# Kernel optimization log

Measured on AMD Instinct MI355X. Metric: run time of the kernel, lower is better.

## Reference

```python
import jax, jax.numpy as jnp
import numpy as np

N = 100000   # nodes
E = 1600000  # edges
D_IN, D_H, D_OUT = 128, 256, 128
EPS = 1e-5


def _linear_params(key, fan_in, fan_out):
    lim = 1.0 / np.sqrt(fan_in)
    kw, kb = jax.random.split(key)
    W = jax.random.uniform(kw, (fan_in, fan_out), minval=-lim, maxval=lim, dtype=jnp.float32)
    b = jax.random.uniform(kb, (fan_out,), minval=-lim, maxval=lim, dtype=jnp.float32)
    return W, b


def setup_inputs() -> dict:
    key = jax.random.key(0)
    ks = jax.random.split(key, 8)
    W1, b1 = _linear_params(ks[0], D_IN, D_H)
    W2, b2 = _linear_params(ks[1], D_H, D_H)
    W3, b3 = _linear_params(ks[2], D_H, D_OUT)
    return {
        'feat': jax.random.normal(ks[3], (N, D_IN), dtype=jnp.float32),
        'W1': W1, 'b1': b1, 'g1': jnp.ones(D_H, jnp.float32), 'be1': jnp.zeros(D_H, jnp.float32), 'a1': jnp.full((1,), 0.25, jnp.float32),
        'W2': W2, 'b2': b2, 'g2': jnp.ones(D_H, jnp.float32), 'be2': jnp.zeros(D_H, jnp.float32), 'a2': jnp.full((1,), 0.25, jnp.float32),
        'W3': W3, 'b3': b3,
        'src': jax.random.randint(ks[4], (E,), 0, N, dtype=jnp.int32),
        'dst': jax.random.randint(ks[5], (E,), 0, N, dtype=jnp.int32),
    }


def _layer_norm(x, g, b):
    mu = jnp.mean(x, axis=-1, keepdims=True)
    var = jnp.mean((x - mu) ** 2, axis=-1, keepdims=True)
    return g * (x - mu) / jnp.sqrt(var + EPS) + b


def _prelu(x, a):
    return jnp.where(x >= 0, x, a * x)


def reference(feat, W1, b1, g1, be1, a1, W2, b2, g2, be2, a2, W3, b3, src, dst):
    ones = jnp.ones((E,), jnp.float32)
    # out-degree (of src nodes) and in-degree (of dst nodes), clamped to >= 1
    deg_out = jnp.maximum(jax.ops.segment_sum(ones, src, num_segments=N), 1.0) ** -0.5  # [N]
    deg_in = jnp.maximum(jax.ops.segment_sum(ones, dst, num_segments=N), 1.0) ** -0.5   # [N]

    def conv(h, W, b, g=None, be=None, a=None):
        x = h * deg_out[:, None]                                   # src-side degree norm
        agg = jax.ops.segment_sum(x[src], dst, num_segments=N)     # sparse sum aggregation
        r = (agg @ W + b) * deg_in[:, None]                        # linear + dst-side norm
        if g is not None:
            r = _prelu(_layer_norm(r, g, be), a)
        return r

    h = conv(feat, W1, b1, g1, be1, a1)
    h = conv(h, W2, b2, g2, be2, a2)
    h = conv(h, W3, b3)  # last layer: encoding=False -> no norm, no activation
    return h
```

## Files before the change

kernel.cpp:

```cpp
#include <hip/hip_runtime.h>
#include <cstdint>
#include <cstddef>

static constexpr int NN = 100000;
static constexpr int NE = 1600000;
static constexpr int NP = 100096;

static constexpr int NBUCK  = 391;
static constexpr int BCAP   = 5120;
static constexpr int NBUCKD = 782;
static constexpr int BCAPD  = 2816;
static constexpr int SCAP   = 448;
static constexpr int PBLK   = 200;
static constexpr int EPB    = 8000;

typedef __attribute__((ext_vector_type(8))) short short8;
typedef __attribute__((ext_vector_type(8))) unsigned short ushort8;
typedef __attribute__((ext_vector_type(4))) float f32x4;

__device__ inline ushort bf16_rtn(float x) {
    uint32_t u = __float_as_uint(x);
    uint32_t r = u + 0x7fffu + ((u >> 16) & 1u);
    return (ushort)(r >> 16);
}
__device__ inline float bf16_to_f(ushort u) {
    return __uint_as_float((uint32_t)u << 16);
}

__global__ __launch_bounds__(256) void k_init_cur(int* __restrict__ curA) {
    int b = blockIdx.x * 256 + threadIdx.x;
    if (b < NBUCK) curA[b] = b * BCAP;
}

__global__ __launch_bounds__(256) void k_partA(const int* __restrict__ src, const int* __restrict__ dst,
                                               int* __restrict__ curA, int* __restrict__ pairA) {
    __shared__ int hs[NBUCK];
    int e0 = blockIdx.x * EPB;
    for (int i = threadIdx.x; i < NBUCK; i += 256) hs[i] = 0;
    __syncthreads();
    for (int e = e0 + (int)threadIdx.x; e < e0 + EPB; e += 256)
        atomicAdd(&hs[src[e] >> 8], 1);
    __syncthreads();
    for (int i = threadIdx.x; i < NBUCK; i += 256) {
        int c = hs[i];
        hs[i] = c ? atomicAdd(&curA[i], c) : 0;
    }
    __syncthreads();
    for (int e = e0 + (int)threadIdx.x; e < e0 + EPB; e += 256) {
        int s = src[e], d = dst[e];
        int p = atomicAdd(&hs[s >> 8], 1);
        pairA[p] = (d << 8) | (s & 255);
    }
}

__global__ __launch_bounds__(256) void k_degout(const int* __restrict__ curA, const int* __restrict__ pairA,
                                                float* __restrict__ deg_out_inv) {
    __shared__ int h[256];
    int b = blockIdx.x;
    int p0 = b * BCAP;
    int n = curA[b] - p0;
    h[threadIdx.x] = 0;
    __syncthreads();
    for (int i = threadIdx.x; i < n; i += 256)
        atomicAdd(&h[pairA[p0 + i] & 255], 1);
    __syncthreads();
    int node = b * 256 + (int)threadIdx.x;
    if (node < NN)
        deg_out_inv[node] = rsqrtf(fmaxf((float)h[threadIdx.x], 1.0f));
}

__global__ __launch_bounds__(256) void k_countB(const int* __restrict__ curA, const int* __restrict__ pairA,
                                                int* __restrict__ cntB) {
    __shared__ int h[NBUCKD];
    int s = blockIdx.x;
    int p0 = s * BCAP;
    int n = curA[s] - p0;
    for (int i = threadIdx.x; i < NBUCKD; i += 256) h[i] = 0;
    __syncthreads();
    for (int i = threadIdx.x; i < n; i += 256)
        atomicAdd(&h[pairA[p0 + i] >> 15], 1);
    __syncthreads();
    for (int i = threadIdx.x; i < NBUCKD; i += 256)
        cntB[s * NBUCKD + i] = h[i];
}

__global__ __launch_bounds__(512) void k_scanB(const int* __restrict__ cntB, int* __restrict__ offB,
                                               int* __restrict__ fillB) {
    __shared__ int sd[512];
    int b = blockIdx.x;
    int t = threadIdx.x;
    int v = (t < NBUCK) ? cntB[t * NBUCKD + b] : 0;
    sd[t] = v;
    __syncthreads();
    #pragma unroll
    for (int off = 1; off < 512; off <<= 1) {
        int x = (t >= off) ? sd[t - off] : 0;
        __syncthreads();
        sd[t] += x;
        __syncthreads();
    }
    if (t < NBUCK) offB[t * NBUCKD + b] = b * BCAPD + sd[t] - v;
    if (t == NBUCK - 1) fillB[b] = sd[t];
}

__global__ __launch_bounds__(256) void k_placeB(const int* __restrict__ curA, const int* __restrict__ pairA,
                                                const int* __restrict__ offB, int* __restrict__ pairB) {
    __shared__ int cur[NBUCKD];
    int s = blockIdx.x;
    int p0 = s * BCAP;
    int n = curA[s] - p0;
    for (int i = threadIdx.x; i < NBUCKD; i += 256) cur[i] = offB[s * NBUCKD + i];
    __syncthreads();
    int sbase = s << 8;
    for (int i = threadIdx.x; i < n; i += 256) {
        int pk = pairA[p0 + i];
        int d = pk >> 8;
        int sfull = sbase | (pk & 255);
        int pos = atomicAdd(&cur[d >> 7], 1);
        pairB[pos] = (sfull << 7) | (d & 127);
    }
}

__global__ __launch_bounds__(256) void k_deg_in(const int* __restrict__ fillB, const int* __restrict__ pairB,
                                                float* __restrict__ deg_in_inv) {
    __shared__ int h[128];
    int b = blockIdx.x;
    int p0 = b * BCAPD;
    int n = fillB[b];
    if (threadIdx.x < 128) h[threadIdx.x] = 0;
    __syncthreads();
    for (int i = threadIdx.x; i < n; i += 256)
        atomicAdd(&h[pairB[p0 + i] & 127], 1);
    __syncthreads();
    if (threadIdx.x < 128) {
        int node = b * 128 + (int)threadIdx.x;
        deg_in_inv[node] = rsqrtf(fmaxf((float)h[threadIdx.x], 1.0f));
    }
}

__global__ __launch_bounds__(512) void k_split8(const int* __restrict__ fillB, const int* __restrict__ pairB,
                                                int* __restrict__ pairB2, int* __restrict__ fillS) {
    int b = blockIdx.x;
    int w = threadIdx.x >> 6;
    int l = threadIdx.x & 63;
    int n = fillB[b];
    const int* ep = pairB + (size_t)b * BCAPD;
    int* op = pairB2 + (size_t)(b * 8 + w) * SCAP;
    int cnt = 0;
    for (int i0 = 0; i0 < n; i0 += 64) {
        int idx = i0 + l;
        int pk = (idx < n) ? ep[idx] : 0;
        bool match = (idx < n) && ((pk & 7) == w);
        unsigned long long mask = __ballot(match);
        if (match) {
            int pos = __popcll(mask & ((1ull << l) - 1ull));
            op[cnt + pos] = pk;
        }
        cnt += __popcll(mask);
    }
    if (l == 0) fillS[b * 8 + w] = cnt;
}

__global__ __launch_bounds__(256) void k_cvt(const float* __restrict__ feat,
                                             const float* __restrict__ deg_out_inv,
                                             ushort* __restrict__ out) {
    int idx = blockIdx.x * 256 + threadIdx.x;
    if (idx >= NN * 32) return;
    float4 v = *(const float4*)(feat + (size_t)idx * 4);
    float w = deg_out_inv[idx >> 5];
    ushort4 o;
    o.x = bf16_rtn(v.x * w);
    o.y = bf16_rtn(v.y * w);
    o.z = bf16_rtn(v.z * w);
    o.w = bf16_rtn(v.w * w);
    *(ushort4*)(out + (size_t)idx * 4) = o;
}

template <int XSTRIDE, int COLOFF, bool FINAL>
__global__ __launch_bounds__(512) void k_agg_push2(const int* __restrict__ pairB2, const int* __restrict__ fillS,
                                                   const ushort* __restrict__ x,
                                                   const float* __restrict__ bias,
                                                   const float* __restrict__ deg_in_inv,
                                                   ushort* __restrict__ out_b, float* __restrict__ out_f) {
    __shared__ float lacc[128 * 128];
    int b = blockIdx.x;
    for (int i = threadIdx.x; i < 4096; i += 512)
        *(float4*)&lacc[i * 4] = (float4){0.f, 0.f, 0.f, 0.f};
    __syncthreads();
    int w = threadIdx.x >> 6;
    int l = threadIdx.x & 63;
    int sb = b * 8 + w;
    int m = fillS[sb];
    const int* ep = pairB2 + (size_t)sb * SCAP;
    const ushort* xb = x + COLOFF + 2 * l;
    int i = 0;
    for (; i + 8 <= m; i += 8) {
        int pk[8];
        #pragma unroll
        for (int j = 0; j < 8; ++j) pk[j] = ep[i + j];
        ushort2 v[8];
        #pragma unroll
        for (int j = 0; j < 8; ++j)
            v[j] = *(const ushort2*)(xb + (size_t)(pk[j] >> 7) * XSTRIDE);
        #pragma unroll
        for (int j = 0; j < 8; ++j) {
            int a = (pk[j] & 127) * 128 + 2 * l;
            float2 c = *(float2*)&lacc[a];
            c.x += bf16_to_f(v[j].x);
            c.y += bf16_to_f(v[j].y);
            *(float2*)&lacc[a] = c;
        }
    }
    for (; i < m; ++i) {
        int pk = ep[i];
        ushort2 vv = *(const ushort2*)(xb + (size_t)(pk >> 7) * XSTRIDE);
        int a = (pk & 127) * 128 + 2 * l;
        float2 c = *(float2*)&lacc[a];
        c.x += bf16_to_f(vv.x);
        c.y += bf16_to_f(vv.y);
        *(float2*)&lacc[a] = c;
    }
    __syncthreads();
    if constexpr (FINAL) {
        float2 bv = *(const float2*)(bias + 2 * l);
        #pragma unroll 4
        for (int rr = 0; rr < 16; ++rr) {
            int rl = w * 16 + rr;
            int node = b * 128 + rl;
            if (node < NN) {
                float dv = deg_in_inv[node];
                float2 c = *(float2*)&lacc[rl * 128 + 2 * l];
                float2 o;
                o.x = (c.x + bv.x) * dv;
                o.y = (c.y + bv.y) * dv;
                *(float2*)(out_f + (size_t)node * 128 + 2 * l) = o;
            }
        }
    } else {
        #pragma unroll 4
        for (int rr = 0; rr < 16; ++rr) {
            int rl = w * 16 + rr;
            int node = b * 128 + rl;
            float2 c = *(float2*)&lacc[rl * 128 + 2 * l];
            ushort2 o;
            o.x = bf16_rtn(c.x);
            o.y = bf16_rtn(c.y);
            *(ushort2*)(out_b + (size_t)node * XSTRIDE + COLOFF + 2 * l) = o;
        }
    }
}

template <int K, int M>
__device__ inline void packW_dev(const float* __restrict__ W, ushort* __restrict__ out, int blk) {
    constexpr int NT = M / 16, KC = K / 32;
    constexpr int WTOT = KC * NT * 512;
    int idx = blk * 256 + (int)threadIdx.x;
    int lane = idx & 63;
    int tile = idx >> 6;
    int nt = tile % NT, kc = tile / NT;
    int col = nt * 16 + (lane & 15);
    int kbase = kc * 32 + (lane >> 4) * 8;
    size_t o = (size_t)tile * 512 + lane * 8;
    #pragma unroll
    for (int j = 0; j < 8; ++j) {
        float w = W[(size_t)(kbase + j) * M + col];
        uint32_t u = __float_as_uint(w);
        uint32_t hu = u & 0xffff0000u;
        float lf = w - __uint_as_float(hu);
        out[o + j] = (ushort)(u >> 16);
        out[o + WTOT + j] = (ushort)(__float_as_uint(lf) >> 16);
    }
}

__global__ __launch_bounds__(256) void k_packAll(const float* __restrict__ W1, ushort* __restrict__ o1,
                                                 const float* __restrict__ W2, ushort* __restrict__ o2,
                                                 const float* __restrict__ W3, ushort* __restrict__ o3) {
    int b = blockIdx.x;
    if (b < 16) packW_dev<128, 256>(W1, o1, b);
    else if (b < 48) packW_dev<256, 256>(W2, o2, b - 16);
    else packW_dev<256, 128>(W3, o3, b - 48);
}

template <int K, int M, int MODE>
__global__ __launch_bounds__(256) void k_gemm_mfma(const ushort* __restrict__ A,
                                                   const ushort* __restrict__ Wp,
                                                   const float* __restrict__ bias,
                                                   const float* __restrict__ deg_in_inv,
                                                   const float* __restrict__ deg_out_inv,
                                                   const float* __restrict__ g,
                                                   const float* __restrict__ be,
                                                   const float* __restrict__ a,
                                                   ushort* __restrict__ out) {
    constexpr int NT = M / 16;
    constexpr int KC = K / 32;
    constexpr int WTOT = KC * NT * 512;
    constexpr int COLW = M / 64;
    constexpr int ROWW = 4 / COLW;
    constexpr int BROWS = 64 * ROWW;
    constexpr int LROW = M + 8;
    constexpr int NRF = BROWS / 16;
    constexpr int RFW = NRF / 4;
    __shared__ ushort sbuf[BROWS * LROW];
    __shared__ float sredS[4][64];
    __shared__ float sredQ[4][64];
    __shared__ float smu[64];
    __shared__ float srs[64];
    static_assert(BROWS * LROW >= 2 * NRF * 512, "staging dbuf must fit in sbuf");

    int lane = threadIdx.x & 63;
    int wave = threadIdx.x >> 6;
    int cw = wave % COLW;
    int rw = wave / COLW;
    int m = lane & 15;
    int quad = lane >> 4;
    int rowb = blockIdx.x * BROWS + rw * 64;

    f32x4 acc[4][4];
    #pragma unroll
    for (int rf = 0; rf < 4; ++rf)
        #pragma unroll
        for (int ct = 0; ct < 4; ++ct) acc[rf][ct] = (f32x4){0.f, 0.f, 0.f, 0.f};

    const size_t arow0 = (size_t)blockIdx.x * BROWS;
    auto stage = [&](int kc, int buf) {
        #pragma unroll
        for (int s = 0; s < RFW; ++s) {
            int rf = wave * RFW + s;
            const ushort* gsrc = A + (arow0 + rf * 16 + m) * K + kc * 32 + quad * 8;
            ushort* ldst = sbuf + (size_t)(buf * NRF + rf) * 512;
            __builtin_amdgcn_global_load_lds(
                (const __attribute__((address_space(1))) unsigned int*)gsrc,
                (__attribute__((address_space(3))) unsigned int*)ldst, 16, 0, 0);
        }
    };
    stage(0, 0);
    __syncthreads();
    for (int kc = 0; kc < KC; ++kc) {
        if (kc + 1 < KC) stage(kc + 1, (kc + 1) & 1);
        const ushort* ab = sbuf + (size_t)((kc & 1) * NRF + rw * 4) * 512 + lane * 8;
        short8 av[4];
        #pragma unroll
        for (int rf = 0; rf < 4; ++rf)
            av[rf] = *(const short8*)(ab + rf * 512);
        const ushort* wb0 = Wp + ((size_t)kc * NT + cw * 4) * 512 + lane * 8;
        #pragma unroll
        for (int ct = 0; ct < 4; ++ct) {
            short8 bh = *(const short8*)(wb0 + ct * 512);
            short8 bl = *(const short8*)(wb0 + WTOT + ct * 512);
            #pragma unroll
            for (int rf = 0; rf < 4; ++rf) {
                acc[rf][ct] = __builtin_amdgcn_mfma_f32_16x16x32_bf16(av[rf], bh, acc[rf][ct], 0, 0, 0);
                acc[rf][ct] = __builtin_amdgcn_mfma_f32_16x16x32_bf16(av[rf], bl, acc[rf][ct], 0, 0, 0);
            }
        }
        __syncthreads();
    }
    if constexpr (MODE == 1) {
        float bia[4];
        #pragma unroll
        for (int ct = 0; ct < 4; ++ct) bia[ct] = bias[cw * 64 + ct * 16 + m];
        float din[4][4], fold[4][4];
        #pragma unroll
        for (int rf = 0; rf < 4; ++rf)
            #pragma unroll
            for (int r = 0; r < 4; ++r) {
                int row = rowb + rf * 16 + quad * 4 + r;
                din[rf][r] = deg_in_inv[row];
                fold[rf][r] = deg_out_inv[row];
            }
        float s[4][4], q[4][4];
        #pragma unroll
        for (int rf = 0; rf < 4; ++rf)
            #pragma unroll
            for (int r = 0; r < 4; ++r) { s[rf][r] = 0.f; q[rf][r] = 0.f; }
        #pragma unroll
        for (int rf = 0; rf < 4; ++rf)
            #pragma unroll
            for (int ct = 0; ct < 4; ++ct)
                #pragma unroll
                for (int r = 0; r < 4; ++r) {
                    float v = (acc[rf][ct][r] + bia[ct]) * din[rf][r];
                    acc[rf][ct][r] = v;
                    s[rf][r] += v;
                    q[rf][r] += v * v;
                }
        #pragma unroll
        for (int w = 1; w < 16; w <<= 1)
            #pragma unroll
            for (int rf = 0; rf < 4; ++rf)
                #pragma unroll
                for (int r = 0; r < 4; ++r) {
                    s[rf][r] += __shfl_xor(s[rf][r], w);
                    q[rf][r] += __shfl_xor(q[rf][r], w);
                }
        if (m == 0) {
            #pragma unroll
            for (int rf = 0; rf < 4; ++rf)
                #pragma unroll
                for (int r = 0; r < 4; ++r) {
                    int rl = rf * 16 + quad * 4 + r;
                    sredS[wave][rl] = s[rf][r];
                    sredQ[wave][rl] = q[rf][r];
                }
        }
        __syncthreads();
        if (threadIdx.x < 64) {
            int rl = threadIdx.x;
            float st = sredS[0][rl] + sredS[1][rl] + sredS[2][rl] + sredS[3][rl];
            float qt = sredQ[0][rl] + sredQ[1][rl] + sredQ[2][rl] + sredQ[3][rl];
            float mu = st * (1.0f / M);
            float var = qt * (1.0f / M) - mu * mu;
            smu[rl] = mu;
            srs[rl] = rsqrtf(var + 1e-5f);
        }
        __syncthreads();
        float alpha = a[0];
        float gv[4], bev[4];
        #pragma unroll
        for (int ct = 0; ct < 4; ++ct) {
            gv[ct] = g[cw * 64 + ct * 16 + m];
            bev[ct] = be[cw * 64 + ct * 16 + m];
        }
        #pragma unroll
        for (int rf = 0; rf < 4; ++rf)
            #pragma unroll
            for (int r = 0; r < 4; ++r) {
                int rl = rf * 16 + quad * 4 + r;
                float mu = smu[rl];
                float rs = srs[rl];
                float fo = fold[rf][r];
                #pragma unroll
                for (int ct = 0; ct < 4; ++ct) {
                    float v = gv[ct] * (acc[rf][ct][r] - mu) * rs + bev[ct];
                    v = (v >= 0.0f) ? v : alpha * v;
                    v *= fo;
                    sbuf[rl * LROW + cw * 64 + ct * 16 + m] = bf16_rtn(v);
                }
            }
    } else {
        #pragma unroll
        for (int rf = 0; rf < 4; ++rf)
            #pragma unroll
            for (int ct = 0; ct < 4; ++ct)
                #pragma unroll
                for (int r = 0; r < 4; ++r)
                    sbuf[(rw * 64 + rf * 16 + quad * 4 + r) * LROW + cw * 64 + ct * 16 + m] =
                        bf16_rtn(acc[rf][ct][r]);
    }
    __syncthreads();
    constexpr int CNT = BROWS * M / 256;
    int trow = ((int)threadIdx.x * CNT) / M;
    int tcol = ((int)threadIdx.x * CNT) % M;
    const ushort* rsrc = sbuf + trow * LROW + tcol;
    ushort* gdst = out + (size_t)(blockIdx.x * BROWS + trow) * M + tcol;
    #pragma unroll
    for (int j = 0; j < CNT / 8; ++j) {
        ushort8 v = *(const ushort8*)(rsrc + j * 8);
        *(ushort8*)(gdst + j * 8) = v;
    }
}

extern "C" void kernel_launch(void* const* d_in, const int* in_sizes, int n_in,
                              void* d_out, int out_size, void* d_ws, size_t ws_size,
                              hipStream_t stream) {
    const float* feat = (const float*)d_in[0];
    const float* W1 = (const float*)d_in[1];
    const float* b1 = (const float*)d_in[2];
    const float* g1 = (const float*)d_in[3];
    const float* be1 = (const float*)d_in[4];
    const float* a1 = (const float*)d_in[5];
    const float* W2 = (const float*)d_in[6];
    const float* b2 = (const float*)d_in[7];
    const float* g2 = (const float*)d_in[8];
    const float* be2 = (const float*)d_in[9];
    const float* a2 = (const float*)d_in[10];
    const float* W3 = (const float*)d_in[11];
    const float* b3 = (const float*)d_in[12];
    const int* src = (const int*)d_in[13];
    const int* dst = (const int*)d_in[14];

    char* ws = (char*)d_ws;
    size_t off = 0;
    auto alloc = [&](size_t bytes) -> void* {
        off = (off + 511) & ~(size_t)511;
        void* p = ws + off;
        off += bytes;
        return p;
    };
    int* curA = (int*)alloc((size_t)NBUCK * 4);
    float* deg_out_inv = (float*)alloc((size_t)NP * 4);
    float* deg_in_inv = (float*)alloc((size_t)NP * 4);
    int* pairA = (int*)alloc((size_t)NBUCK * BCAP * 4);
    int* pairB = (int*)alloc((size_t)NBUCKD * BCAPD * 4);
    int* pairB2 = (int*)alloc((size_t)NBUCKD * 8 * SCAP * 4);
    int* fillS = (int*)alloc((size_t)NBUCKD * 8 * 4);
    int* cntB = (int*)alloc((size_t)NBUCK * NBUCKD * 4);
    int* offB = (int*)alloc((size_t)NBUCK * NBUCKD * 4);
    int* fillB = (int*)alloc((size_t)NBUCKD * 4);
    ushort* Wp1 = (ushort*)alloc((size_t)2 * 4 * 16 * 512 * 2);
    ushort* Wp2 = (ushort*)alloc((size_t)2 * 8 * 16 * 512 * 2);
    ushort* Wp3 = (ushort*)alloc((size_t)2 * 8 * 8 * 512 * 2);
    ushort* featb = (ushort*)alloc((size_t)NP * 128 * 2);
    ushort* aggb  = (ushort*)alloc((size_t)NP * 256 * 2);
    ushort* hb    = (ushort*)alloc((size_t)NP * 256 * 2);
    ushort* yb    = (ushort*)alloc((size_t)NP * 128 * 2);
    (void)ws_size; (void)in_sizes; (void)n_in; (void)out_size;

    k_init_cur<<<2, 256, 0, stream>>>(curA);
    k_partA<<<PBLK, 256, 0, stream>>>(src, dst, curA, pairA);
    k_degout<<<NBUCK, 256, 0, stream>>>(curA, pairA, deg_out_inv);
    k_countB<<<NBUCK, 256, 0, stream>>>(curA, pairA, cntB);
    k_scanB<<<NBUCKD, 512, 0, stream>>>(cntB, offB, fillB);
    k_placeB<<<NBUCK, 256, 0, stream>>>(curA, pairA, offB, pairB);
    k_deg_in<<<NBUCKD, 256, 0, stream>>>(fillB, pairB, deg_in_inv);
    k_split8<<<NBUCKD, 512, 0, stream>>>(fillB, pairB, pairB2, fillS);

    k_packAll<<<64, 256, 0, stream>>>(W1, Wp1, W2, Wp2, W3, Wp3);
    k_cvt<<<(NN * 32 + 255) / 256, 256, 0, stream>>>(feat, deg_out_inv, featb);

    k_agg_push2<128, 0, false><<<NBUCKD, 512, 0, stream>>>(pairB2, fillS, featb, nullptr, nullptr, aggb, nullptr);
    k_gemm_mfma<128, 256, 1><<<NP / 64, 256, 0, stream>>>(aggb, Wp1, b1, deg_in_inv, deg_out_inv, g1, be1, a1, hb);

    k_agg_push2<256, 0, false><<<NBUCKD, 512, 0, stream>>>(pairB2, fillS, hb, nullptr, nullptr, aggb, nullptr);
    k_agg_push2<256, 128, false><<<NBUCKD, 512, 0, stream>>>(pairB2, fillS, hb, nullptr, nullptr, aggb, nullptr);
    k_gemm_mfma<256, 256, 1><<<NP / 64, 256, 0, stream>>>(aggb, Wp2, b2, deg_in_inv, deg_out_inv, g2, be2, a2, hb);

    k_gemm_mfma<256, 128, 0><<<NP / 128, 256, 0, stream>>>(hb, Wp3, nullptr, nullptr, nullptr, nullptr, nullptr, nullptr, yb);
    k_agg_push2<128, 0, true><<<NBUCKD, 512, 0, stream>>>(pairB2, fillS, yb, b3, deg_in_inv, nullptr, (float*)d_out);
}
```

Measured before the change: 680.1 us.

## Split dst buckets into 32 sub-lists and aggregate with 1024-thread half-wave groups

The edge split kernel now divides each destination bucket into 32 sub-lists (by dst & 31) instead of 8, staging the bucket in shared memory first. The aggregation kernel runs 1024 threads, and each 32-lane group handles one sub-list using 8-byte ushort4 gathers, int4 edge-index loads and float4 LDS accumulation. The epilogue writes 16 contiguous columns per thread with vector stores. This gives more parallel gather streams and wider memory accesses. The risks are the smaller per-sub-list capacity of 128 (possible overflow on skewed degree distributions), int4 reads of up to three padding entries past the fill count (masked out by zero weights), and 1024-thread blocks that limit occupancy to one block per 64KB of LDS.

```diff
diff --git a/kernel.cpp b/kernel.cpp
--- a/kernel.cpp
+++ b/kernel.cpp
@@ -10,7 +10,7 @@
 static constexpr int BCAP   = 5120;
 static constexpr int NBUCKD = 782;
 static constexpr int BCAPD  = 2816;
-static constexpr int SCAP   = 448;
+static constexpr int SCAP   = 128;
 static constexpr int PBLK   = 200;
 static constexpr int EPB    = 8000;
 
@@ -138,27 +138,33 @@
     }
 }
 
-__global__ __launch_bounds__(512) void k_split8(const int* __restrict__ fillB, const int* __restrict__ pairB,
-                                                int* __restrict__ pairB2, int* __restrict__ fillS) {
+__global__ __launch_bounds__(512) void k_split32(const int* __restrict__ fillB, const int* __restrict__ pairB,
+                                                 int* __restrict__ pairB2, int* __restrict__ fillS) {
+    __shared__ int se[BCAPD];
     int b = blockIdx.x;
+    int n = fillB[b];
+    const int* ep = pairB + (size_t)b * BCAPD;
+    for (int i = threadIdx.x; i < n; i += 512) se[i] = ep[i];
+    __syncthreads();
     int w = threadIdx.x >> 6;
     int l = threadIdx.x & 63;
-    int n = fillB[b];
-    const int* ep = pairB + (size_t)b * BCAPD;
-    int* op = pairB2 + (size_t)(b * 8 + w) * SCAP;
-    int cnt = 0;
-    for (int i0 = 0; i0 < n; i0 += 64) {
-        int idx = i0 + l;
-        int pk = (idx < n) ? ep[idx] : 0;
-        bool match = (idx < n) && ((pk & 7) == w);
-        unsigned long long mask = __ballot(match);
-        if (match) {
-            int pos = __popcll(mask & ((1ull << l) - 1ull));
-            op[cnt + pos] = pk;
-        }
-        cnt += __popcll(mask);
-    }
-    if (l == 0) fillS[b * 8 + w] = cnt;
+    for (int r = 0; r < 4; ++r) {
+        int h = w + 8 * r;
+        int* op = pairB2 + (size_t)(b * 32 + h) * SCAP;
+        int cnt = 0;
+        for (int i0 = 0; i0 < n; i0 += 64) {
+            int idx = i0 + l;
+            int pk = (idx < n) ? se[idx] : 0;
+            bool match = (idx < n) && ((pk & 31) == h);
+            unsigned long long mask = __ballot(match);
+            if (match) {
+                int pos = __popcll(mask & ((1ull << l) - 1ull));
+                op[cnt + pos] = pk;
+            }
+            cnt += __popcll(mask);
+        }
+        if (l == 0) fillS[b * 32 + h] = cnt;
+    }
 }
 
 __global__ __launch_bounds__(256) void k_cvt(const float* __restrict__ feat,
@@ -177,76 +183,76 @@
 }
 
 template <int XSTRIDE, int COLOFF, bool FINAL>
-__global__ __launch_bounds__(512) void k_agg_push2(const int* __restrict__ pairB2, const int* __restrict__ fillS,
-                                                   const ushort* __restrict__ x,
-                                                   const float* __restrict__ bias,
-                                                   const float* __restrict__ deg_in_inv,
-                                                   ushort* __restrict__ out_b, float* __restrict__ out_f) {
+__global__ __launch_bounds__(1024) void k_agg_push3(const int* __restrict__ pairB2, const int* __restrict__ fillS,
+                                                    const ushort* __restrict__ x,
+                                                    const float* __restrict__ bias,
+                                                    const float* __restrict__ deg_in_inv,
+                                                    ushort* __restrict__ out_b, float* __restrict__ out_f) {
     __shared__ float lacc[128 * 128];
     int b = blockIdx.x;
-    for (int i = threadIdx.x; i < 4096; i += 512)
+    for (int i = threadIdx.x; i < 4096; i += 1024)
         *(float4*)&lacc[i * 4] = (float4){0.f, 0.f, 0.f, 0.f};
     __syncthreads();
-    int w = threadIdx.x >> 6;
-    int l = threadIdx.x & 63;
-    int sb = b * 8 + w;
+    int h = threadIdx.x >> 5;
+    int l5 = threadIdx.x & 31;
+    int sb = b * 32 + h;
     int m = fillS[sb];
     const int* ep = pairB2 + (size_t)sb * SCAP;
-    const ushort* xb = x + COLOFF + 2 * l;
-    int i = 0;
-    for (; i + 8 <= m; i += 8) {
-        int pk[8];
-        #pragma unroll
-        for (int j = 0; j < 8; ++j) pk[j] = ep[i + j];
-        ushort2 v[8];
-        #pragma unroll
-        for (int j = 0; j < 8; ++j)
-            v[j] = *(const ushort2*)(xb + (size_t)(pk[j] >> 7) * XSTRIDE);
-        #pragma unroll
-        for (int j = 0; j < 8; ++j) {
-            int a = (pk[j] & 127) * 128 + 2 * l;
-            float2 c = *(float2*)&lacc[a];
-            c.x += bf16_to_f(v[j].x);
-            c.y += bf16_to_f(v[j].y);
-            *(float2*)&lacc[a] = c;
-        }
-    }
-    for (; i < m; ++i) {
-        int pk = ep[i];
-        ushort2 vv = *(const ushort2*)(xb + (size_t)(pk >> 7) * XSTRIDE);
-        int a = (pk & 127) * 128 + 2 * l;
-        float2 c = *(float2*)&lacc[a];
-        c.x += bf16_to_f(vv.x);
-        c.y += bf16_to_f(vv.y);
-        *(float2*)&lacc[a] = c;
-    }
-    __syncthreads();
+    const ushort* xb = x + COLOFF + l5 * 4;
+    for (int i0 = 0; i0 < m; i0 += 4) {
+        int4 pks = *(const int4*)(ep + i0);
+        int pk[4] = {pks.x, pks.y, pks.z, pks.w};
+        ushort4 v[4];
+        float wt[4];
+        #pragma unroll
+        for (int j = 0; j < 4; ++j) {
+            bool ok = (i0 + j < m);
+            wt[j] = ok ? 1.0f : 0.0f;
+            pk[j] = ok ? pk[j] : pk[0];
+            v[j] = *(const ushort4*)(xb + (size_t)(pk[j] >> 7) * XSTRIDE);
+        }
+        #pragma unroll
+        for (int j = 0; j < 4; ++j) {
+            int a = (pk[j] & 127) * 128 + l5 * 4;
+            float4 c = *(float4*)&lacc[a];
+            c.x += wt[j] * bf16_to_f(v[j].x);
+            c.y += wt[j] * bf16_to_f(v[j].y);
+            c.z += wt[j] * bf16_to_f(v[j].z);
+            c.w += wt[j] * bf16_to_f(v[j].w);
+            *(float4*)&lacc[a] = c;
+        }
+    }
+    __syncthreads();
+    int row = threadIdx.x >> 3;
+    int cg = threadIdx.x & 7;
+    int node = b * 128 + row;
+    const float* lp = &lacc[row * 128 + cg * 16];
     if constexpr (FINAL) {
-        float2 bv = *(const float2*)(bias + 2 * l);
-        #pragma unroll 4
-        for (int rr = 0; rr < 16; ++rr) {
-            int rl = w * 16 + rr;
-            int node = b * 128 + rl;
-            if (node < NN) {
-                float dv = deg_in_inv[node];
-                float2 c = *(float2*)&lacc[rl * 128 + 2 * l];
-                float2 o;
+        if (node < NN) {
+            float dv = deg_in_inv[node];
+            float* op = out_f + (size_t)node * 128 + cg * 16;
+            #pragma unroll
+            for (int gq = 0; gq < 4; ++gq) {
+                float4 c = *(const float4*)(lp + gq * 4);
+                float4 bv = *(const float4*)(bias + cg * 16 + gq * 4);
+                float4 o;
                 o.x = (c.x + bv.x) * dv;
                 o.y = (c.y + bv.y) * dv;
-                *(float2*)(out_f + (size_t)node * 128 + 2 * l) = o;
+                o.z = (c.z + bv.z) * dv;
+                o.w = (c.w + bv.w) * dv;
+                *(float4*)(op + gq * 4) = o;
             }
         }
     } else {
-        #pragma unroll 4
-        for (int rr = 0; rr < 16; ++rr) {
-            int rl = w * 16 + rr;
-            int node = b * 128 + rl;
-            float2 c = *(float2*)&lacc[rl * 128 + 2 * l];
-            ushort2 o;
-            o.x = bf16_rtn(c.x);
-            o.y = bf16_rtn(c.y);
-            *(ushort2*)(out_b + (size_t)node * XSTRIDE + COLOFF + 2 * l) = o;
-        }
+        ushort8 u0, u1;
+        #pragma unroll
+        for (int k = 0; k < 8; ++k) {
+            u0[k] = bf16_rtn(lp[k]);
+            u1[k] = bf16_rtn(lp[8 + k]);
+        }
+        ushort* op = out_b + (size_t)node * XSTRIDE + COLOFF + cg * 16;
+        *(ushort8*)op = u0;
+        *(ushort8*)(op + 8) = u1;
     }
 }
 
@@ -492,8 +498,8 @@
     float* deg_in_inv = (float*)alloc((size_t)NP * 4);
     int* pairA = (int*)alloc((size_t)NBUCK * BCAP * 4);
     int* pairB = (int*)alloc((size_t)NBUCKD * BCAPD * 4);
-    int* pairB2 = (int*)alloc((size_t)NBUCKD * 8 * SCAP * 4);
-    int* fillS = (int*)alloc((size_t)NBUCKD * 8 * 4);
+    int* pairB2 = (int*)alloc((size_t)NBUCKD * 32 * SCAP * 4);
+    int* fillS = (int*)alloc((size_t)NBUCKD * 32 * 4);
     int* cntB = (int*)alloc((size_t)NBUCK * NBUCKD * 4);
     int* offB = (int*)alloc((size_t)NBUCK * NBUCKD * 4);
     int* fillB = (int*)alloc((size_t)NBUCKD * 4);
@@ -513,18 +519,18 @@
     k_scanB<<<NBUCKD, 512, 0, stream>>>(cntB, offB, fillB);
     k_placeB<<<NBUCK, 256, 0, stream>>>(curA, pairA, offB, pairB);
     k_deg_in<<<NBUCKD, 256, 0, stream>>>(fillB, pairB, deg_in_inv);
-    k_split8<<<NBUCKD, 512, 0, stream>>>(fillB, pairB, pairB2, fillS);
+    k_split32<<<NBUCKD, 512, 0, stream>>>(fillB, pairB, pairB2, fillS);
 
     k_packAll<<<64, 256, 0, stream>>>(W1, Wp1, W2, Wp2, W3, Wp3);
     k_cvt<<<(NN * 32 + 255) / 256, 256, 0, stream>>>(feat, deg_out_inv, featb);
 
-    k_agg_push2<128, 0, false><<<NBUCKD, 512, 0, stream>>>(pairB2, fillS, featb, nullptr, nullptr, aggb, nullptr);
+    k_agg_push3<128, 0, false><<<NBUCKD, 1024, 0, stream>>>(pairB2, fillS, featb, nullptr, nullptr, aggb, nullptr);
     k_gemm_mfma<128, 256, 1><<<NP / 64, 256, 0, stream>>>(aggb, Wp1, b1, deg_in_inv, deg_out_inv, g1, be1, a1, hb);
 
-    k_agg_push2<256, 0, false><<<NBUCKD, 512, 0, stream>>>(pairB2, fillS, hb, nullptr, nullptr, aggb, nullptr);
-    k_agg_push2<256, 128, false><<<NBUCKD, 512, 0, stream>>>(pairB2, fillS, hb, nullptr, nullptr, aggb, nullptr);
+    k_agg_push3<256, 0, false><<<NBUCKD, 1024, 0, stream>>>(pairB2, fillS, hb, nullptr, nullptr, aggb, nullptr);
+    k_agg_push3<256, 128, false><<<NBUCKD, 1024, 0, stream>>>(pairB2, fillS, hb, nullptr, nullptr, aggb, nullptr);
     k_gemm_mfma<256, 256, 1><<<NP / 64, 256, 0, stream>>>(aggb, Wp2, b2, deg_in_inv, deg_out_inv, g2, be2, a2, hb);
 
     k_gemm_mfma<256, 128, 0><<<NP / 128, 256, 0, stream>>>(hb, Wp3, nullptr, nullptr, nullptr, nullptr, nullptr, nullptr, yb);
-    k_agg_push2<128, 0, true><<<NBUCKD, 512, 0, stream>>>(pairB2, fillS, yb, b3, deg_in_inv, nullptr, (float*)d_out);
-}
+    k_agg_push3<128, 0, true><<<NBUCKD, 1024, 0, stream>>>(pairB2, fillS, yb, b3, deg_in_inv, nullptr, (float*)d_out);
+}
```

After: 638.4 us. 1.07x faster.
